# Performance work log

Hardware: AMD Instinct MI355X
Metric: run time of the kernel (lower is better)

Reference implementation:

```python
import jax, jax.numpy as jnp
import numpy as np

B, C, T, H, W = 8, 128, 16, 32, 32
M, N, CS = 64, 64, 64


def setup_inputs() -> dict:
    key = jax.random.key(0)
    ks = jax.random.split(key, 12)
    s = 0.02
    return {
        "input": jax.random.normal(ks[0], (B, C, T, H, W), dtype=jnp.float32),
        "condition": jax.random.normal(ks[1], (B, CS), dtype=jnp.float32),
        # 1x1x1 Conv3d weights collapse to (out, in) matrices
        "W_phi": jax.random.normal(ks[2], (M, C), dtype=jnp.float32) * s,
        "b_phi": jax.random.normal(ks[3], (M,), dtype=jnp.float32) * s,
        "W_theta": jax.random.normal(ks[4], (N, C), dtype=jnp.float32) * s,
        "b_theta": jax.random.normal(ks[5], (N,), dtype=jnp.float32) * s,
        "W_rho": jax.random.normal(ks[6], (N, C), dtype=jnp.float32) * s,
        "b_rho": jax.random.normal(ks[7], (N,), dtype=jnp.float32) * s,
        "W1": jax.random.normal(ks[8], (CS, CS), dtype=jnp.float32) * s,
        "b1": jax.random.normal(ks[9], (CS,), dtype=jnp.float32) * s,
        "W2": jax.random.normal(ks[10], (H * W, CS), dtype=jnp.float32) * s,
        "b2": jax.random.normal(ks[11], (H * W,), dtype=jnp.float32) * s,
    }


def _pointwise_conv3d(x, Wt, b):
    # Conv3d with kernel=1, stride=1 == channel mixing
    return jnp.einsum('bcthw,oc->bothw', x, Wt) + b[None, :, None, None, None]


def reference(input, condition, W_phi, b_phi, W_theta, b_theta, W_rho, b_rho, W1, b1, W2, b2):
    x = input.reshape(-1, C, T, H, W)
    cond = condition.reshape(x.shape[0], -1)
    A = _pointwise_conv3d(x, W_phi, b_phi)                       # (b,m,t,h,w)
    B0 = _pointwise_conv3d(x, W_theta, b_theta)                  # (b,n,t,h,w)
    Bm = jax.nn.softmax(B0.reshape(B0.shape[0], B0.shape[1], -1), axis=-1).reshape(B0.shape)
    # FC_Cond: Linear+ReLU, Linear+ReLU, then softmax over h*w
    h1 = jax.nn.relu(cond @ W1.T + b1)
    h2 = jax.nn.relu(h1 @ W2.T + b2)
    Cm = jax.nn.softmax(h2, axis=-1).reshape(-1, H, W)           # (b,h,w)
    BC = Bm * Cm[:, None, None, :, :]                            # (b,n,t,h,w)
    AB_T = jnp.einsum('bmthw,bnthw->bmn', A, BC)                 # (b,m,n)
    V = jax.nn.softmax(_pointwise_conv3d(x, W_rho, b_rho), axis=1)
    Z = jnp.einsum('bmn,bnthw->bmthw', AB_T, V)
    attn = jnp.transpose(Bm * V, (0, 1, 3, 4, 2))                # (b,n,h,w,t)
    return (Z, attn)
```

## Files before the change

kernel.cpp:

```cpp
#include <hip/hip_runtime.h>

#define CC 128
#define SB 16384

typedef _Float16 half4_t __attribute__((ext_vector_type(4)));
typedef _Float16 half8_t __attribute__((ext_vector_type(8)));
typedef float    f32x4  __attribute__((ext_vector_type(4)));

#define WH_OFF   0u
#define ABH_OFF  0u
#define BIAS_OFF 49152u
#define CM_OFF   50176u
#define SUME_OFF 82944u
#define XT_OFF   262144u
#define VT_OFF   33816576u

__global__ void k0_setup(const float* __restrict__ cond,
                         const float* __restrict__ W_phi, const float* __restrict__ b_phi,
                         const float* __restrict__ W_theta, const float* __restrict__ b_theta,
                         const float* __restrict__ W_rho, const float* __restrict__ b_rho,
                         const float* __restrict__ W1, const float* __restrict__ b1,
                         const float* __restrict__ W2, const float* __restrict__ b2,
                         char* __restrict__ wsc) {
  __shared__ float sc[64], sh1[64], red[256];
  int t = threadIdx.x, bid = blockIdx.x;
  if (bid < 8) {
    int b = bid;
    if (t < 64) sc[t] = cond[b*64 + t];
    __syncthreads();
    if (t < 64) {
      float acc = b1[t];
      for (int k = 0; k < 64; ++k) acc += sc[k] * W1[t*64 + k];
      sh1[t] = fmaxf(acc, 0.f);
    }
    __syncthreads();
    float ev[4]; float ps = 0.f;
    #pragma unroll
    for (int q = 0; q < 4; ++q) {
      int o = q*256 + t;
      float acc = b2[o];
      for (int k = 0; k < 64; ++k) acc += sh1[k] * W2[o*64 + k];
      ev[q] = __expf(fmaxf(acc, 0.f));
      ps += ev[q];
    }
    red[t] = ps; __syncthreads();
    for (int s = 128; s > 0; s >>= 1) { if (t < s) red[t] += red[t+s]; __syncthreads(); }
    float inv = 1.f / red[0];
    float* cm = (float*)(wsc + CM_OFF);
    #pragma unroll
    for (int q = 0; q < 4; ++q) cm[b*1024 + q*256 + t] = ev[q] * inv;
  } else {
    int r = bid - 8;
    _Float16* wh = (_Float16*)(wsc + WH_OFF);
    for (int i = r*256 + t; i < 24576; i += 2048) {
      int set = i >> 13, mk = i & 8191;
      const float* W = (set == 0) ? W_phi : (set == 1 ? W_theta : W_rho);
      wh[i] = (_Float16)W[mk];
    }
    if (r == 0 && t < 192) {
      float* bias = (float*)(wsc + BIAS_OFF);
      bias[t] = (t < 64) ? b_phi[t] : (t < 128 ? b_theta[t-64] : b_rho[t-128]);
    }
    if (r == 1) {
      float* se = (float*)(wsc + SUME_OFF);
      for (int i = t; i < 512; i += 256) se[i] = 0.f;
    }
  }
}

__global__ __launch_bounds__(256, 2) void kT_transpose(const float* __restrict__ x,
                                                       _Float16* __restrict__ xt) {
  __shared__ float Xs[128*133];
  int t = threadIdx.x, bid = blockIdx.x;
  int b = bid >> 7, chunk = bid & 127;
  int s0 = chunk * 128;
  const float* xb = x + (size_t)b*CC*SB + s0;
  #pragma unroll
  for (int r = 0; r < 16; ++r) {
    int fid = r*256 + t;
    int c = fid >> 5, s4 = (fid & 31) << 2;
    *(float4*)&Xs[c*133 + s4] = *(const float4*)(xb + (size_t)c*SB + s4);
  }
  __syncthreads();
  int c8 = t & 15, sl = t >> 4;
  _Float16* xo = xt + ((size_t)b*SB + s0)*128 + c8*8;
  #pragma unroll
  for (int it = 0; it < 8; ++it) {
    int s = it*16 + sl;
    half8_t h;
    #pragma unroll
    for (int i = 0; i < 8; ++i) h[i] = (_Float16)Xs[(c8*8 + i)*133 + s];
    *(half8_t*)(xo + (size_t)s*128) = h;
  }
}

__global__ __launch_bounds__(256, 2) void kC_main(
    const _Float16* __restrict__ xt, const _Float16* __restrict__ wh,
    const float* __restrict__ bias, const float* __restrict__ cm,
    float* __restrict__ sumE, _Float16* __restrict__ vt,
    char* __restrict__ ptb,
    float* __restrict__ part) {
  __shared__ _Float16 Xt_l[128*136];
  __shared__ _Float16 A_l[64*136];
  __shared__ _Float16 E_l[64*136];
  __shared__ float se_l[256];

  int t = threadIdx.x;
  int lane = t & 63, wv = t >> 6, ln = lane & 15, q = lane >> 4;
  int bid = blockIdx.x, b = bid >> 7, chunk = bid & 127;
  int s0 = chunk * 128;

  #pragma unroll
  for (int r = 0; r < 8; ++r) {
    int fid = r*256 + t;
    int s = fid >> 4, c16 = fid & 15;
    *(half8_t*)&Xt_l[s*136 + c16*8] =
        *(const half8_t*)(xt + ((size_t)b*SB + s0 + s)*128 + c16*8);
  }
  __syncthreads();

  half8_t bf[2][4];
  int myp = wv * 32;
  #pragma unroll
  for (int nt = 0; nt < 2; ++nt)
    #pragma unroll
    for (int kk = 0; kk < 4; ++kk)
      bf[nt][kk] = *(half8_t*)&Xt_l[(myp + nt*16 + ln)*136 + kk*32 + q*8];

  int gsl[2] = { s0 + myp + ln, s0 + myp + 16 + ln };
  float cmv[2] = { cm[b*1024 + (gsl[0] & 1023)], cm[b*1024 + (gsl[1] & 1023)] };

  half8_t af[4][4];
  f32x4 d[4][2];
  float ev[4][2][4];

  auto conv = [&](int setoff) {
    #pragma unroll
    for (int mt = 0; mt < 4; ++mt)
      #pragma unroll
      for (int kk = 0; kk < 4; ++kk)
        af[mt][kk] = *(const half8_t*)(wh + setoff + (mt*16 + ln)*128 + kk*32 + q*8);
    #pragma unroll
    for (int mt = 0; mt < 4; ++mt)
      #pragma unroll
      for (int nt = 0; nt < 2; ++nt)
        d[mt][nt] = (f32x4){0.f, 0.f, 0.f, 0.f};
    #pragma unroll
    for (int kk = 0; kk < 4; ++kk)
      #pragma unroll
      for (int mt = 0; mt < 4; ++mt)
        #pragma unroll
        for (int nt = 0; nt < 2; ++nt)
          d[mt][nt] = __builtin_amdgcn_mfma_f32_16x16x32_f16(af[mt][kk], bf[nt][kk],
                                                             d[mt][nt], 0, 0, 0);
  };

  conv(0);
  #pragma unroll
  for (int mt = 0; mt < 4; ++mt) {
    float bv[4]; *(float4*)bv = *(const float4*)(bias + mt*16 + q*4);
    #pragma unroll
    for (int nt = 0; nt < 2; ++nt)
      #pragma unroll
      for (int r = 0; r < 4; ++r)
        A_l[(mt*16 + q*4 + r)*136 + myp + nt*16 + ln] = (_Float16)(d[mt][nt][r] + bv[r]);
  }

  conv(8192);
  float sp[4][4];
  #pragma unroll
  for (int mt = 0; mt < 4; ++mt) {
    float bv[4]; *(float4*)bv = *(const float4*)(bias + 64 + mt*16 + q*4);
    #pragma unroll
    for (int r = 0; r < 4; ++r) {
      #pragma unroll
      for (int nt = 0; nt < 2; ++nt) {
        float e = __expf(d[mt][nt][r] + bv[r]);
        ev[mt][nt][r] = e;
        E_l[(mt*16 + q*4 + r)*136 + myp + nt*16 + ln] = (_Float16)(e * cmv[nt]);
      }
      sp[mt][r] = ev[mt][0][r] + ev[mt][1][r];
    }
  }
  #pragma unroll
  for (int mt = 0; mt < 4; ++mt)
    #pragma unroll
    for (int r = 0; r < 4; ++r) {
      float v = sp[mt][r];
      v += __shfl_xor(v, 1); v += __shfl_xor(v, 2);
      v += __shfl_xor(v, 4); v += __shfl_xor(v, 8);
      sp[mt][r] = v;
    }
  if (ln == 0) {
    #pragma unroll
    for (int mt = 0; mt < 4; ++mt)
      #pragma unroll
      for (int r = 0; r < 4; ++r)
        se_l[wv*64 + mt*16 + q*4 + r] = sp[mt][r];
  }

  conv(16384);
  #pragma unroll
  for (int mt = 0; mt < 4; ++mt) {
    float bv[4]; *(float4*)bv = *(const float4*)(bias + 128 + mt*16 + q*4);
    #pragma unroll
    for (int nt = 0; nt < 2; ++nt)
      #pragma unroll
      for (int r = 0; r < 4; ++r)
        d[mt][nt][r] = __expf(d[mt][nt][r] + bv[r]);
  }
  float cs[2] = {0.f, 0.f};
  #pragma unroll
  for (int mt = 0; mt < 4; ++mt)
    #pragma unroll
    for (int nt = 0; nt < 2; ++nt)
      #pragma unroll
      for (int r = 0; r < 4; ++r) cs[nt] += d[mt][nt][r];
  #pragma unroll
  for (int nt = 0; nt < 2; ++nt) {
    cs[nt] += __shfl_xor(cs[nt], 16);
    cs[nt] += __shfl_xor(cs[nt], 32);
    cs[nt] = 1.f / cs[nt];
  }
  #pragma unroll
  for (int nt = 0; nt < 2; ++nt) {
    size_t grow = (size_t)b*SB + gsl[nt];
    _Float16* vrow = vt + grow*64;
    char* prow = ptb + grow*256 + 128;
    #pragma unroll
    for (int mt = 0; mt < 4; ++mt) {
      half4_t hv, hp;
      #pragma unroll
      for (int r = 0; r < 4; ++r) {
        float vv = d[mt][nt][r] * cs[nt];
        hv[r] = (_Float16)vv;
        hp[r] = (_Float16)(vv * ev[mt][nt][r]);
      }
      *(half4_t*)(vrow + mt*16 + q*4) = hv;
      *(half4_t*)(prow + (size_t)(mt*16 + q*4)*2) = hp;
    }
  }
  __syncthreads();

  if (t < 64) {
    float ssum = se_l[t] + se_l[64+t] + se_l[128+t] + se_l[192+t];
    atomicAdd(&sumE[b*64 + t], ssum);
  }

  f32x4 dab[4];
  #pragma unroll
  for (int n2 = 0; n2 < 4; ++n2) dab[n2] = (f32x4){0.f, 0.f, 0.f, 0.f};
  #pragma unroll
  for (int kk = 0; kk < 4; ++kk) {
    half8_t aab = *(half8_t*)&A_l[(wv*16 + ln)*136 + kk*32 + q*8];
    #pragma unroll
    for (int n2 = 0; n2 < 4; ++n2) {
      half8_t bab = *(half8_t*)&E_l[(n2*16 + ln)*136 + kk*32 + q*8];
      dab[n2] = __builtin_amdgcn_mfma_f32_16x16x32_f16(aab, bab, dab[n2], 0, 0, 0);
    }
  }
  float* pp = part + (size_t)bid*4096;
  #pragma unroll
  for (int n2 = 0; n2 < 4; ++n2)
    #pragma unroll
    for (int r = 0; r < 4; ++r)
      pp[(wv*16 + q*4 + r)*64 + n2*16 + ln] = dab[n2][r];
}

__global__ void k2_reduce(const float* __restrict__ part, const float* __restrict__ sumE,
                          _Float16* __restrict__ abh) {
  int idx = blockIdx.x*256 + threadIdx.x;
  int b = idx >> 12, mn = idx & 4095, n = mn & 63;
  const float* p = part + (size_t)b*128*4096 + mn;
  float s = 0.f;
  #pragma unroll 4
  for (int k = 0; k < 128; ++k) s += p[(size_t)k*4096];
  abh[idx] = (_Float16)(s * (1024.f / sumE[b*64 + n]));
}

__global__ __launch_bounds__(256) void k3_z(const _Float16* __restrict__ abh,
                                            const _Float16* __restrict__ vt,
                                            float* __restrict__ zout) {
  __shared__ _Float16 Ah[64*72];
  int t = threadIdx.x;
  int lane = t & 63, wv = t >> 6, ln = lane & 15, q = lane >> 4;
  int bid = blockIdx.x, b = bid >> 6, chunk = bid & 63;
  int s0 = chunk * 256;
  #pragma unroll
  for (int r = 0; r < 2; ++r) {
    int fid = r*256 + t;
    int m = fid >> 3, n8 = fid & 7;
    *(half8_t*)&Ah[m*72 + n8*8] = *(const half8_t*)(abh + b*4096 + m*64 + n8*8);
  }
  __syncthreads();
  half8_t a8[4][2];
  #pragma unroll
  for (int mt = 0; mt < 4; ++mt)
    #pragma unroll
    for (int kk = 0; kk < 2; ++kk)
      a8[mt][kk] = *(half8_t*)&Ah[(mt*16 + ln)*72 + kk*32 + q*8];
  int sw = s0 + wv*64;
  #pragma unroll
  for (int nt = 0; nt < 4; ++nt) {
    int sb = sw + nt*16 + ln;
    const _Float16* vrow = vt + ((size_t)b*SB + sb)*64;
    half8_t b8[2];
    b8[0] = *(const half8_t*)(vrow + q*8);
    b8[1] = *(const half8_t*)(vrow + 32 + q*8);
    f32x4 dz[4];
    #pragma unroll
    for (int mt = 0; mt < 4; ++mt) dz[mt] = (f32x4){0.f, 0.f, 0.f, 0.f};
    #pragma unroll
    for (int kk = 0; kk < 2; ++kk)
      #pragma unroll
      for (int mt = 0; mt < 4; ++mt)
        dz[mt] = __builtin_amdgcn_mfma_f32_16x16x32_f16(a8[mt][kk], b8[kk], dz[mt], 0, 0, 0);
    #pragma unroll
    for (int mt = 0; mt < 4; ++mt)
      #pragma unroll
      for (int r = 0; r < 4; ++r)
        zout[((size_t)(b*64 + mt*16 + q*4 + r))*SB + sb] = dz[mt][r] * (1.f/1024.f);
  }
}

__global__ __launch_bounds__(256) void k4_attn(const char* __restrict__ ptb,
                                               const float* __restrict__ sumE,
                                               float* __restrict__ outA) {
  __shared__ _Float16 P_l[256*72];
  int t = threadIdx.x, bid = blockIdx.x;
  int b = bid >> 6, hw0 = (bid & 63) * 16;
  int st = t >> 4, h = t & 15;
  int s = st*1024 + hw0 + h;
  const char* prow = ptb + ((size_t)b*SB + s)*256 + 128;
  #pragma unroll
  for (int c8 = 0; c8 < 8; ++c8)
    *(half8_t*)&P_l[t*72 + c8*8] = *(const half8_t*)(prow + c8*16);
  __syncthreads();
  int n = t >> 2, oc = t & 3;
  float ri = 1.f / sumE[b*64 + n];
  float* orow = outA + 8388608 + (size_t)(b*64 + n)*SB + hw0*16;
  #pragma unroll
  for (int i = 0; i < 16; ++i) {
    int j = oc*64 + i*4;
    int hh = j >> 4, stb = j & 15;
    float w[4];
    #pragma unroll
    for (int r = 0; r < 4; ++r)
      w[r] = (float)P_l[((stb + r)*16 + hh)*72 + n] * ri;
    *(float4*)(orow + j) = *(float4*)w;
  }
}

extern "C" void kernel_launch(void* const* d_in, const int* in_sizes, int n_in,
                              void* d_out, int out_size, void* d_ws, size_t ws_size,
                              hipStream_t stream) {
  const float* input   = (const float*)d_in[0];
  const float* cond    = (const float*)d_in[1];
  const float* W_phi   = (const float*)d_in[2];
  const float* b_phi   = (const float*)d_in[3];
  const float* W_theta = (const float*)d_in[4];
  const float* b_theta = (const float*)d_in[5];
  const float* W_rho   = (const float*)d_in[6];
  const float* b_rho   = (const float*)d_in[7];
  const float* W1      = (const float*)d_in[8];
  const float* b1      = (const float*)d_in[9];
  const float* W2      = (const float*)d_in[10];
  const float* b2      = (const float*)d_in[11];
  char* wsc = (char*)d_ws;
  float* out = (float*)d_out;

  const _Float16* wh = (const _Float16*)(wsc + WH_OFF);
  _Float16* abh  = (_Float16*)(wsc + ABH_OFF);
  const float* bias = (const float*)(wsc + BIAS_OFF);
  const float* cmp  = (const float*)(wsc + CM_OFF);
  float* sumE  = (float*)(wsc + SUME_OFF);
  _Float16* xt = (_Float16*)(wsc + XT_OFF);
  _Float16* vt = (_Float16*)(wsc + VT_OFF);
  float* part  = out + 8388608;

  hipLaunchKernelGGL(k0_setup, dim3(16), dim3(256), 0, stream,
                     cond, W_phi, b_phi, W_theta, b_theta, W_rho, b_rho,
                     W1, b1, W2, b2, wsc);
  hipLaunchKernelGGL(kT_transpose, dim3(1024), dim3(256), 0, stream, input, xt);
  hipLaunchKernelGGL(kC_main, dim3(1024), dim3(256), 0, stream,
                     xt, wh, bias, cmp, sumE, vt, (char*)(wsc + XT_OFF), part);
  hipLaunchKernelGGL(k2_reduce, dim3(128), dim3(256), 0, stream, part, sumE, abh);
  hipLaunchKernelGGL(k3_z, dim3(512), dim3(256), 0, stream, abh, vt, out);
  hipLaunchKernelGGL(k4_attn, dim3(512), dim3(256), 0, stream,
                     (const char*)(wsc + XT_OFF), sumE, out);
}
```

Before: 227.9 us.

## Fuse input transpose into main kernel and shrink shared memory for occupancy

Removes the separate transpose kernel that wrote a half-precision channel-last copy of the input to global memory. The main kernel now reads fp32 input directly, transposes it in four staged passes through a small padded shared buffer, and aliases shared buffers so occupancy can rise to 3 blocks per CU. The P intermediate gets its own compact buffer instead of living interleaved in the old transpose region. This saves a full global write and re-read of the transposed input, at the cost of extra barriers and strided fp32 loads inside the main kernel.

```diff
diff --git a/kernel.cpp b/kernel.cpp
--- a/kernel.cpp
+++ b/kernel.cpp
@@ -12,8 +12,8 @@
 #define BIAS_OFF 49152u
 #define CM_OFF   50176u
 #define SUME_OFF 82944u
-#define XT_OFF   262144u
-#define VT_OFF   33816576u
+#define PT_OFF   262144u
+#define VT_OFF   17039360u
 
 __global__ void k0_setup(const float* __restrict__ cond,
                          const float* __restrict__ W_phi, const float* __restrict__ b_phi,
@@ -68,56 +68,44 @@
   }
 }
 
-__global__ __launch_bounds__(256, 2) void kT_transpose(const float* __restrict__ x,
-                                                       _Float16* __restrict__ xt) {
-  __shared__ float Xs[128*133];
-  int t = threadIdx.x, bid = blockIdx.x;
-  int b = bid >> 7, chunk = bid & 127;
-  int s0 = chunk * 128;
-  const float* xb = x + (size_t)b*CC*SB + s0;
-  #pragma unroll
-  for (int r = 0; r < 16; ++r) {
-    int fid = r*256 + t;
-    int c = fid >> 5, s4 = (fid & 31) << 2;
-    *(float4*)&Xs[c*133 + s4] = *(const float4*)(xb + (size_t)c*SB + s4);
-  }
-  __syncthreads();
-  int c8 = t & 15, sl = t >> 4;
-  _Float16* xo = xt + ((size_t)b*SB + s0)*128 + c8*8;
-  #pragma unroll
-  for (int it = 0; it < 8; ++it) {
-    int s = it*16 + sl;
-    half8_t h;
-    #pragma unroll
-    for (int i = 0; i < 8; ++i) h[i] = (_Float16)Xs[(c8*8 + i)*133 + s];
-    *(half8_t*)(xo + (size_t)s*128) = h;
-  }
-}
-
-__global__ __launch_bounds__(256, 2) void kC_main(
-    const _Float16* __restrict__ xt, const _Float16* __restrict__ wh,
+__global__ __launch_bounds__(256, 3) void kC_main(
+    const float* __restrict__ x, const _Float16* __restrict__ wh,
     const float* __restrict__ bias, const float* __restrict__ cm,
     float* __restrict__ sumE, _Float16* __restrict__ vt,
-    char* __restrict__ ptb,
-    float* __restrict__ part) {
-  __shared__ _Float16 Xt_l[128*136];
-  __shared__ _Float16 A_l[64*136];
-  __shared__ _Float16 E_l[64*136];
-  __shared__ float se_l[256];
+    _Float16* __restrict__ pt, float* __restrict__ part) {
+  __shared__ char smraw[52736];
+  _Float16* Xt_l = (_Float16*)smraw;
+  float*    Xs   = (float*)(smraw + 34816);
+  _Float16* A_l  = (_Float16*)smraw;
+  _Float16* E_l  = (_Float16*)(smraw + 17408);
+  float*    se_l = (float*)(smraw + 51712);
 
   int t = threadIdx.x;
   int lane = t & 63, wv = t >> 6, ln = lane & 15, q = lane >> 4;
   int bid = blockIdx.x, b = bid >> 7, chunk = bid & 127;
   int s0 = chunk * 128;
-
-  #pragma unroll
-  for (int r = 0; r < 8; ++r) {
-    int fid = r*256 + t;
-    int s = fid >> 4, c16 = fid & 15;
-    *(half8_t*)&Xt_l[s*136 + c16*8] =
-        *(const half8_t*)(xt + ((size_t)b*SB + s0 + s)*128 + c16*8);
-  }
-  __syncthreads();
+  const float* xb = x + (size_t)b*CC*SB + s0;
+
+  #pragma unroll
+  for (int st = 0; st < 4; ++st) {
+    #pragma unroll
+    for (int r = 0; r < 4; ++r) {
+      int fid = r*256 + t;
+      int c = fid >> 3, s4 = (fid & 7) << 2;
+      *(float4*)&Xs[c*33 + s4] = *(const float4*)(xb + (size_t)c*SB + st*32 + s4);
+    }
+    __syncthreads();
+    #pragma unroll
+    for (int r = 0; r < 2; ++r) {
+      int fid = r*256 + t;
+      int s = fid >> 4, c8 = fid & 15;
+      half8_t h;
+      #pragma unroll
+      for (int i = 0; i < 8; ++i) h[i] = (_Float16)Xs[(c8*8 + i)*33 + s];
+      *(half8_t*)&Xt_l[(st*32 + s)*136 + c8*8] = h;
+    }
+    __syncthreads();
+  }
 
   half8_t bf[2][4];
   int myp = wv * 32;
@@ -126,6 +114,7 @@
     #pragma unroll
     for (int kk = 0; kk < 4; ++kk)
       bf[nt][kk] = *(half8_t*)&Xt_l[(myp + nt*16 + ln)*136 + kk*32 + q*8];
+  __syncthreads();
 
   int gsl[2] = { s0 + myp + ln, s0 + myp + 16 + ln };
   float cmv[2] = { cm[b*1024 + (gsl[0] & 1023)], cm[b*1024 + (gsl[1] & 1023)] };
@@ -226,7 +215,7 @@
   for (int nt = 0; nt < 2; ++nt) {
     size_t grow = (size_t)b*SB + gsl[nt];
     _Float16* vrow = vt + grow*64;
-    char* prow = ptb + grow*256 + 128;
+    _Float16* prow = pt + grow*64;
     #pragma unroll
     for (int mt = 0; mt < 4; ++mt) {
       half4_t hv, hp;
@@ -237,7 +226,7 @@
         hp[r] = (_Float16)(vv * ev[mt][nt][r]);
       }
       *(half4_t*)(vrow + mt*16 + q*4) = hv;
-      *(half4_t*)(prow + (size_t)(mt*16 + q*4)*2) = hp;
+      *(half4_t*)(prow + mt*16 + q*4) = hp;
     }
   }
   __syncthreads();
@@ -323,7 +312,7 @@
   }
 }
 
-__global__ __launch_bounds__(256) void k4_attn(const char* __restrict__ ptb,
+__global__ __launch_bounds__(256) void k4_attn(const _Float16* __restrict__ pt,
                                                const float* __restrict__ sumE,
                                                float* __restrict__ outA) {
   __shared__ _Float16 P_l[256*72];
@@ -331,10 +320,10 @@
   int b = bid >> 6, hw0 = (bid & 63) * 16;
   int st = t >> 4, h = t & 15;
   int s = st*1024 + hw0 + h;
-  const char* prow = ptb + ((size_t)b*SB + s)*256 + 128;
+  const _Float16* prow = pt + ((size_t)b*SB + s)*64;
   #pragma unroll
   for (int c8 = 0; c8 < 8; ++c8)
-    *(half8_t*)&P_l[t*72 + c8*8] = *(const half8_t*)(prow + c8*16);
+    *(half8_t*)&P_l[t*72 + c8*8] = *(const half8_t*)(prow + c8*8);
   __syncthreads();
   int n = t >> 2, oc = t & 3;
   float ri = 1.f / sumE[b*64 + n];
@@ -374,18 +363,16 @@
   const float* bias = (const float*)(wsc + BIAS_OFF);
   const float* cmp  = (const float*)(wsc + CM_OFF);
   float* sumE  = (float*)(wsc + SUME_OFF);
-  _Float16* xt = (_Float16*)(wsc + XT_OFF);
+  _Float16* pt = (_Float16*)(wsc + PT_OFF);
   _Float16* vt = (_Float16*)(wsc + VT_OFF);
   float* part  = out + 8388608;
 
   hipLaunchKernelGGL(k0_setup, dim3(16), dim3(256), 0, stream,
                      cond, W_phi, b_phi, W_theta, b_theta, W_rho, b_rho,
                      W1, b1, W2, b2, wsc);
-  hipLaunchKernelGGL(kT_transpose, dim3(1024), dim3(256), 0, stream, input, xt);
   hipLaunchKernelGGL(kC_main, dim3(1024), dim3(256), 0, stream,
-                     xt, wh, bias, cmp, sumE, vt, (char*)(wsc + XT_OFF), part);
+                     input, wh, bias, cmp, sumE, vt, pt, part);
   hipLaunchKernelGGL(k2_reduce, dim3(128), dim3(256), 0, stream, part, sumE, abh);
   hipLaunchKernelGGL(k3_z, dim3(512), dim3(256), 0, stream, abh, vt, out);
-  hipLaunchKernelGGL(k4_attn, dim3(512), dim3(256), 0, stream,
-                     (const char*)(wsc + XT_OFF), sumE, out);
-}
+  hipLaunchKernelGGL(k4_attn, dim3(512), dim3(256), 0, stream, pt, sumE, out);
+}
```

Measured after the change: 235.4 us. 3.3% more time.
